# Kernel optimization log

Hardware: AMD Instinct MI355X
Metric: run time of the kernel (lower is better)

## Reference

```python
import jax, jax.numpy as jnp
import numpy as np

QTZ_BETA = 0.25


def setup_inputs() -> dict:
    key = jax.random.key(0)
    k1, k2 = jax.random.split(key)
    z = jax.random.normal(k1, (65536, 1, 256), dtype=jnp.float32)
    codebook = jax.random.normal(k2, (4096, 256), dtype=jnp.float32)
    return {"z": z, "codebook": codebook}


def reference(z, codebook):
    """Hard VQ quantization: nearest-codebook lookup with straight-through
    estimator plus codebook commitment loss. Returns (z_q, codebook_loss,
    min_embed_ids)."""
    D = codebook.shape[-1]
    z_f = z.reshape(-1, D)  # [N, D]
    # Pairwise squared L2 distances via expansion: ||z||^2 - 2 z c^T + ||c||^2
    # (argmin is invariant to the monotone transform vs. torch.cdist's sqrt)
    d2 = (
        jnp.sum(z_f * z_f, axis=1, keepdims=True)  # [N, 1]
        - 2.0 * (z_f @ codebook.T)                 # [N, K]
        + jnp.sum(codebook * codebook, axis=1)     # [K]
    )
    min_embed_ids = jnp.argmin(d2, axis=1)  # [N]
    # one_hot @ codebook is exactly a gather of codebook rows
    z_q = jnp.take(codebook, min_embed_ids, axis=0).reshape(z.shape)
    # Straight-through estimator
    z_q = z + jax.lax.stop_gradient(z_q - z)
    # Codebook loss (uses the STE z_q, matching the torch code)
    codebook_loss = (
        jnp.mean((jax.lax.stop_gradient(z_q) - z) ** 2)
        + jnp.mean((z_q - jax.lax.stop_gradient(z)) ** 2) * QTZ_BETA
    )
    return (z_q, codebook_loss, min_embed_ids)
```

## Files before the change

kernel.cpp:

```cpp
#include <hip/hip_runtime.h>
#include <stdint.h>

typedef _Float16 f16;
typedef _Float16 f16x4 __attribute__((ext_vector_type(4)));
typedef _Float16 f16x8 __attribute__((ext_vector_type(8)));
typedef float f32x4 __attribute__((ext_vector_type(4)));
typedef unsigned long long u64;

#define D_DIM 256
#define K_CB 4096
#define N_ROWS 65536
#define BM 128
#define BN 256
#define N_TILES 16
#define N_STEPS 128
#define LOSS_OFF 16777216
#define IDS_OFF 16777217
#define MAX_FIX 4096

#define WS_CHI 0
#define WS_CN 2097152
#define WS_CNT 2113536
#define WS_ROWS 2113600
#define WS_SLOTS 2129984

#define A_BASE 0
#define B_BASE 65536
#define CN_BASE 131072
#define LDS_BYTES 147456

#define GL_LDS(g, s_) __builtin_amdgcn_global_load_lds( \
    (const __attribute__((address_space(1))) void*)(g), \
    (__attribute__((address_space(3))) void*)(s_), 16, 0, 0)

static __device__ __forceinline__ uint32_t f2u(float x) { union { float f; uint32_t u; } c; c.f = x; return c.u; }
static __device__ __forceinline__ float u2f(uint32_t x) { union { float f; uint32_t u; } c; c.u = x; return c.f; }
static __device__ __forceinline__ uint32_t umin_(uint32_t a, uint32_t b) { return a < b ? a : b; }
static __device__ __forceinline__ uint32_t umax_(uint32_t a, uint32_t b) { return a > b ? a : b; }
static __device__ __forceinline__ u64 d2u(double x) { union { double d; u64 u; } c; c.d = x; return c.u; }

static __device__ __forceinline__ uint32_t med3u(uint32_t a, uint32_t b, uint32_t c) {
    uint32_t d;
    asm("v_med3_u32 %0, %1, %2, %3" : "=v"(d) : "v"(a), "v"(b), "v"(c));
    return d;
}
static __device__ __forceinline__ uint32_t min3u(uint32_t a, uint32_t b, uint32_t c) {
    uint32_t d;
    asm("v_min3_u32 %0, %1, %2, %3" : "=v"(d) : "v"(a), "v"(b), "v"(c));
    return d;
}

#define INS3(s_, kk_) do { \
    const uint32_t kkv_ = (kk_); \
    const uint32_t n1_ = umin_(k1[s_], kkv_); \
    const uint32_t n2_ = med3u(kkv_, k1[s_], k2[s_]); \
    const uint32_t n3_ = med3u(kkv_, k2[s_], k3[s_]); \
    k1[s_] = n1_; k2[s_] = n2_; k3[s_] = n3_; \
} while (0)

__global__ __launch_bounds__(256) void k_prep_cb(const float* __restrict__ cb,
                                                 f16* __restrict__ chi,
                                                 float* __restrict__ cn,
                                                 uint32_t* __restrict__ cnt,
                                                 u64* __restrict__ slots,
                                                 float* __restrict__ loss_slot) {
    const int tid = threadIdx.x;
    const int w = tid >> 6, l = tid & 63;
    const int row = blockIdx.x * 4 + w;
    const float4 v = ((const float4*)cb)[row * 64 + l];
    f16x4 h4;
    h4[0] = (f16)v.x; h4[1] = (f16)v.y; h4[2] = (f16)v.z; h4[3] = (f16)v.w;
    float ss = v.x * v.x + v.y * v.y + v.z * v.z + v.w * v.w;
#pragma unroll
    for (int m = 32; m >= 1; m >>= 1) ss += __shfl_xor(ss, m);
    ((f16x4*)chi)[row * 64 + l] = h4;
    if (l == 0) cn[row] = ss;
    if (tid < 4) slots[blockIdx.x * 4 + tid] = 0xFFFFFFFFFFFFFFFFull;
    if (blockIdx.x == 0 && tid == 0) { *cnt = 0; *loss_slot = 0.0f; }
}

__global__ __launch_bounds__(512, 2) void k_main(const float* __restrict__ z,
                                                 const float* __restrict__ cb,
                                                 const f16* __restrict__ chi,
                                                 const float* __restrict__ cn,
                                                 uint32_t* __restrict__ cnt,
                                                 uint32_t* __restrict__ rows,
                                                 float* __restrict__ out) {
    extern __shared__ char smem[];
    const int tid = threadIdx.x;
    const int w = tid >> 6, l = tid & 63;
    const int wm = w >> 2, wn = w & 3;
    const int l15 = l & 15, qh = l >> 4;
    const int blk = blockIdx.x;
    const float* ztile = z + (size_t)blk * (BM * D_DIM);

    const int e_lo = (w << 4) + (l >> 2);
    const int swq = ((l & 3) ^ ((l >> 3) & 3)) << 3;
    const int offE0 = e_lo * 256 + swq;
    const int offE1 = offE0 + 32768;
    const int stg0 = w * 1024;
    const int stg1 = stg0 + 8192;

#pragma unroll
    for (int s = 0; s < 3; ++s) {
        const f16* gh = chi + s * 32;
        GL_LDS(gh + offE0, smem + B_BASE + s * 16384 + stg0);
        GL_LDS(gh + offE1, smem + B_BASE + s * 16384 + stg1);
    }

    ((float4*)(smem + CN_BASE))[tid] = ((const float4*)cn)[tid];
    ((float4*)(smem + CN_BASE))[tid + 512] = ((const float4*)cn)[tid + 512];

#pragma unroll 4
    for (int p = 0; p < 16; ++p) {
        const int r = p * 8 + w;
        const float4 v = ((const float4*)ztile)[r * 64 + l];
        f16x4 h4;
        h4[0] = (f16)(v.x * -2.0f); h4[1] = (f16)(v.y * -2.0f);
        h4[2] = (f16)(v.z * -2.0f); h4[3] = (f16)(v.w * -2.0f);
        const int kcw = l >> 3, q = (l >> 1) & 3, half = l & 1;
        const int addr = A_BASE + kcw * 8192 + r * 64 + (((q ^ ((r >> 1) & 3))) << 4) + half * 8;
        *(f16x4*)(smem + addr) = h4;
    }

    const int ab = A_BASE + wm * 4096 + l15 * 64 + ((qh ^ ((l15 >> 1) & 3)) << 4);
    const int bb0 = B_BASE + wn * 4096 + l15 * 64 + ((qh ^ ((l15 >> 1) & 3)) << 4);

    uint32_t k1[16], k2[16], k3[16];
#pragma unroll
    for (int s = 0; s < 16; ++s) { k1[s] = 0xFFFFFFFFu; k2[s] = 0xFFFFFFFFu; k3[s] = 0xFFFFFFFFu; }

    f32x4 acc[4][4];
    f16x8 pA[4], pB[4], qA[4], qB[4];

    __syncthreads();

#pragma unroll
    for (int i = 0; i < 4; ++i) pA[i] = *(const f16x8*)(smem + ab + i * 1024);
#pragma unroll
    for (int j = 0; j < 4; ++j) pB[j] = *(const f16x8*)(smem + bb0 + j * 1024);

#define K_STEP(kc_, CA, CB, NA, NB) do { \
    asm volatile("s_waitcnt vmcnt(2)" ::: "memory"); \
    __builtin_amdgcn_s_barrier(); \
    __builtin_amdgcn_sched_barrier(0); \
    { int s3 = tile * 8 + (kc_) + 3; if (s3 > N_STEPS - 1) s3 = N_STEPS - 1; \
      const f16* gh_ = chi + (s3 >> 3) * (BN * D_DIM) + (s3 & 7) * 32; \
      char* bb_ = smem + B_BASE + (((kc_) + 3) & 3) * 16384; \
      GL_LDS(gh_ + offE0, bb_ + stg0); \
      GL_LDS(gh_ + offE1, bb_ + stg1); } \
    _Pragma("unroll") for (int i = 0; i < 4; ++i) \
        NA[i] = *(const f16x8*)(smem + ab + (((kc_) + 1) & 7) * 8192 + i * 1024); \
    _Pragma("unroll") for (int j = 0; j < 4; ++j) \
        NB[j] = *(const f16x8*)(smem + bb0 + (((kc_) + 1) & 3) * 16384 + j * 1024); \
    _Pragma("unroll") for (int i = 0; i < 4; ++i) \
        _Pragma("unroll") for (int j = 0; j < 4; ++j) \
            acc[i][j] = __builtin_amdgcn_mfma_f32_16x16x32_f16(CA[i], CB[j], acc[i][j], 0, 0, 0); \
} while (0)

    for (int tile = 0; tile < N_TILES; ++tile) {
        const int cnb = CN_BASE + tile * 1024 + wn * 256 + l15 * 4;
#pragma unroll
        for (int j = 0; j < 4; ++j) {
            const float base = *(const float*)(smem + cnb + j * 64) + 64.0f;
#pragma unroll
            for (int i = 0; i < 4; ++i) acc[i][j] = (f32x4){base, base, base, base};
        }
        K_STEP(0, pA, pB, qA, qB);
        K_STEP(1, qA, qB, pA, pB);
        K_STEP(2, pA, pB, qA, qB);
        K_STEP(3, qA, qB, pA, pB);
        K_STEP(4, pA, pB, qA, qB);
        K_STEP(5, qA, qB, pA, pB);
        K_STEP(6, pA, pB, qA, qB);
        K_STEP(7, qA, qB, pA, pB);
        const int colb = tile * BN + wn * 64 + l15;
#pragma unroll
        for (int j = 0; j < 4; ++j) {
            const uint32_t col = (uint32_t)(colb + j * 16);
#pragma unroll
            for (int i = 0; i < 4; ++i)
#pragma unroll
                for (int rr = 0; rr < 4; ++rr) {
                    const uint32_t kk = (f2u(acc[i][j][rr]) & 0xFFFFF000u) | col;
                    INS3(i * 4 + rr, kk);
                }
        }
    }
#undef K_STEP
    asm volatile("s_waitcnt vmcnt(0)" ::: "memory");

#pragma unroll
    for (int s = 0; s < 16; ++s) {
        uint32_t a1 = k1[s], a2 = k2[s], a3 = k3[s];
#pragma unroll
        for (int m = 1; m <= 8; m <<= 1) {
            const uint32_t b1 = (uint32_t)__shfl_xor((int)a1, m);
            const uint32_t b2 = (uint32_t)__shfl_xor((int)a2, m);
            const uint32_t b3 = (uint32_t)__shfl_xor((int)a3, m);
            const uint32_t r1 = umin_(a1, b1);
            const uint32_t r2 = min3u(a2, b2, umax_(a1, b1));
            const uint32_t r3 = min3u(umax_(a1, b2), umax_(a2, b1), umin_(a3, b3));
            a1 = r1; a2 = r2; a3 = r3;
        }
        k1[s] = a1; k2[s] = a2; k3[s] = a3;
    }
    __syncthreads();
    uint32_t* mk = (uint32_t*)(smem + CN_BASE);
    double* lossW = (double*)(smem + CN_BASE + 1536);
    if (wn == 0 && l15 == 0) {
#pragma unroll
        for (int s = 0; s < 16; ++s) {
            const int row = wm * 64 + (s >> 2) * 16 + qh * 4 + (s & 3);
            mk[row] = k1[s]; mk[128 + row] = k2[s]; mk[256 + row] = k3[s];
        }
    }
#pragma unroll
    for (int mw = 1; mw < 4; ++mw) {
        __syncthreads();
        if (wn == mw && l15 == 0) {
#pragma unroll
            for (int s = 0; s < 16; ++s) {
                const int row = wm * 64 + (s >> 2) * 16 + qh * 4 + (s & 3);
                const uint32_t b1 = mk[row], b2 = mk[128 + row], b3 = mk[256 + row];
                mk[row] = umin_(k1[s], b1);
                mk[128 + row] = min3u(k2[s], b2, umax_(k1[s], b1));
                mk[256 + row] = min3u(umax_(k1[s], b2), umax_(k2[s], b1), umin_(k3[s], b3));
            }
        }
    }
    __syncthreads();

    double lossAcc = 0.0;
    for (int it = 0; it < 16; ++it) {
        const int row = it * 8 + w;
        const uint32_t K1 = mk[row], K2 = mk[128 + row], K3 = mk[256 + row];
        const int col1 = (int)(K1 & 4095u), col2 = (int)(K2 & 4095u);
        const float4 c1 = ((const float4*)cb)[col1 * 64 + l];
        const float4 c2 = ((const float4*)cb)[col2 * 64 + l];
        const float4 z4 = ((const float4*)ztile)[row * 64 + l];
        double e1, e2;
        {
            const double dx1 = (double)c1.x - z4.x, dy1 = (double)c1.y - z4.y;
            const double dz1 = (double)c1.z - z4.z, dw1 = (double)c1.w - z4.w;
            e1 = dx1 * dx1 + dy1 * dy1 + dz1 * dz1 + dw1 * dw1;
            const double dx2 = (double)c2.x - z4.x, dy2 = (double)c2.y - z4.y;
            const double dz2 = (double)c2.z - z4.z, dw2 = (double)c2.w - z4.w;
            e2 = dx2 * dx2 + dy2 * dy2 + dz2 * dz2 + dw2 * dw2;
        }
        float zn2 = z4.x * z4.x + z4.y * z4.y + z4.z * z4.z + z4.w * z4.w;
#pragma unroll
        for (int m = 32; m >= 1; m >>= 1) {
            e1 += __shfl_xor(e1, m);
            e2 += __shfl_xor(e2, m);
            zn2 += __shfl_xor(zn2, m);
        }
        const bool take1 = (e1 < e2) || (e1 == e2 && col1 <= col2);
        const float4 cw = take1 ? c1 : c2;
        ((float4*)out)[(blk * BM + row) * 64 + l] = cw;
        if (l == 0) {
            const int colw = take1 ? col1 : col2;
            const double ew = take1 ? e1 : e2;
            out[IDS_OFF + blk * BM + row] = (float)colw;
            lossAcc += ew;
            const float d3 = u2f(K3 & 0xFFFFF000u) + zn2 - 64.0f;
            const float eps = 0.006f * sqrtf(zn2) + 0.01f;
            if (!((float)ew < d3 - eps)) {
                const uint32_t e = atomicAdd(cnt, 1u);
                if (e < MAX_FIX) rows[e] = (uint32_t)(blk * BM + row);
            }
        }
    }
    if (l == 0) lossW[w] = lossAcc;
    __syncthreads();
    if (tid == 0) {
        double tot = 0.0;
#pragma unroll
        for (int i = 0; i < 8; ++i) tot += lossW[i];
        atomicAdd(out + LOSS_OFF, (float)(tot * (1.25 / 16777216.0)));
    }
}

__global__ __launch_bounds__(256) void k_fix_scan(const float* __restrict__ z,
                                                  const float* __restrict__ cb,
                                                  const uint32_t* __restrict__ cnt,
                                                  const uint32_t* __restrict__ rows,
                                                  u64* __restrict__ slots) {
    __shared__ float zrow[256];
    __shared__ u64 wmin[4];
    const int tid = threadIdx.x;
    const int w = tid >> 6, l = tid & 63;
    const int chunk = blockIdx.x & 15;
    uint32_t n = *cnt; if (n > MAX_FIX) n = MAX_FIX;
    for (uint32_t e = blockIdx.x >> 4; e < n; e += 64) {
        const int row = (int)rows[e];
        __syncthreads();
        if (tid < 64) ((float4*)zrow)[tid] = ((const float4*)z)[row * 64 + tid];
        __syncthreads();
        const int c = chunk * 256 + tid;
        const float4* crow = (const float4*)(cb + (size_t)c * 256);
        double s = 0.0;
        for (int q = 0; q < 64; ++q) {
            const float4 cv = crow[q];
            const float4 zv = ((const float4*)zrow)[q];
            const double dx = (double)cv.x - zv.x, dy = (double)cv.y - zv.y;
            const double dz = (double)cv.z - zv.z, dw = (double)cv.w - zv.w;
            s += dx * dx + dy * dy + dz * dz + dw * dw;
        }
        u64 key = (d2u(s) & 0xFFFFFFFFFFFFF000ull) | (u64)c;
#pragma unroll
        for (int m = 32; m >= 1; m >>= 1) {
            const u64 o = __shfl_xor(key, m);
            if (o < key) key = o;
        }
        if (l == 0) wmin[w] = key;
        __syncthreads();
        if (tid == 0) {
            u64 k = wmin[0];
            if (wmin[1] < k) k = wmin[1];
            if (wmin[2] < k) k = wmin[2];
            if (wmin[3] < k) k = wmin[3];
            atomicMin(&slots[e], k);
        }
    }
}

__global__ __launch_bounds__(256) void k_fix_patch(const float* __restrict__ z,
                                                   const float* __restrict__ cb,
                                                   const uint32_t* __restrict__ cnt,
                                                   const uint32_t* __restrict__ rows,
                                                   const u64* __restrict__ slots,
                                                   float* __restrict__ out) {
    const int tid = threadIdx.x;
    uint32_t n = *cnt; if (n > MAX_FIX) n = MAX_FIX;
    for (uint32_t e = blockIdx.x; e < n; e += 256) {
        const int row = (int)rows[e];
        const int newc = (int)(slots[e] & 4095ull);
        const int oldc = (int)out[IDS_OFF + row];
        if (newc == oldc) continue;
        double dOld = 0.0, dNew = 0.0;
        if (tid < 64) {
            const float4 zv = ((const float4*)z)[row * 64 + tid];
            const float4 co = ((const float4*)cb)[oldc * 64 + tid];
            const float4 cn4 = ((const float4*)cb)[newc * 64 + tid];
            const double ax = (double)co.x - zv.x, ay = (double)co.y - zv.y;
            const double az = (double)co.z - zv.z, aw = (double)co.w - zv.w;
            dOld = ax * ax + ay * ay + az * az + aw * aw;
            const double bx = (double)cn4.x - zv.x, by = (double)cn4.y - zv.y;
            const double bz = (double)cn4.z - zv.z, bw = (double)cn4.w - zv.w;
            dNew = bx * bx + by * by + bz * bz + bw * bw;
            ((float4*)out)[row * 64 + tid] = cn4;
        }
#pragma unroll
        for (int m = 32; m >= 1; m >>= 1) {
            dOld += __shfl_xor(dOld, m);
            dNew += __shfl_xor(dNew, m);
        }
        if (tid == 0) {
            out[IDS_OFF + row] = (float)newc;
            atomicAdd(out + LOSS_OFF, (float)((dNew - dOld) * (1.25 / 16777216.0)));
        }
    }
}

extern "C" void kernel_launch(void* const* d_in, const int* in_sizes, int n_in,
                              void* d_out, int out_size, void* d_ws, size_t ws_size,
                              hipStream_t stream) {
    (void)in_sizes; (void)n_in; (void)out_size; (void)ws_size;
    const float* z = (const float*)d_in[0];
    const float* cb = (const float*)d_in[1];
    float* out = (float*)d_out;
    char* ws = (char*)d_ws;
    f16* chi = (f16*)(ws + WS_CHI);
    float* cn = (float*)(ws + WS_CN);
    uint32_t* cnt = (uint32_t*)(ws + WS_CNT);
    uint32_t* rows = (uint32_t*)(ws + WS_ROWS);
    u64* slots = (u64*)(ws + WS_SLOTS);

    hipFuncSetAttribute((const void*)k_main,
                        hipFuncAttributeMaxDynamicSharedMemorySize, LDS_BYTES);

    k_prep_cb<<<K_CB / 4, 256, 0, stream>>>(cb, chi, cn, cnt, slots, out + LOSS_OFF);
    k_main<<<N_ROWS / BM, 512, LDS_BYTES, stream>>>(z, cb, chi, cn, cnt, rows, out);
    k_fix_scan<<<1024, 256, 0, stream>>>(z, cb, cnt, rows, slots);
    k_fix_patch<<<256, 256, 0, stream>>>(z, cb, cnt, rows, slots, out);
}
```

Before: 296.0 us.

## Double-buffer accumulators to overlap top-3 epilogue with next tile's MFMAs

After: 305.5 us. 3.2% more time.

```diff
diff --git a/kernel.cpp b/kernel.cpp
--- a/kernel.cpp
+++ b/kernel.cpp
@@ -125,56 +125,86 @@
 
     const int ab = A_BASE + wm * 4096 + l15 * 64 + ((qh ^ ((l15 >> 1) & 3)) << 4);
     const int bb0 = B_BASE + wn * 4096 + l15 * 64 + ((qh ^ ((l15 >> 1) & 3)) << 4);
+    const int cnA = CN_BASE + wn * 256 + l15 * 4;
 
     uint32_t k1[16], k2[16], k3[16];
 #pragma unroll
     for (int s = 0; s < 16; ++s) { k1[s] = 0xFFFFFFFFu; k2[s] = 0xFFFFFFFFu; k3[s] = 0xFFFFFFFFu; }
 
-    f32x4 acc[4][4];
-    f16x8 pA[4], pB[4], qA[4], qB[4];
+    f32x4 accA[4][4], accB[4][4];
+    {
+        const float iv = __builtin_inff();
+#pragma unroll
+        for (int i = 0; i < 4; ++i)
+#pragma unroll
+            for (int j = 0; j < 4; ++j) accB[i][j] = (f32x4){iv, iv, iv, iv};
+    }
+    f16x8 ah[4], bhf[4];
+    float cnNext[4];
 
     __syncthreads();
 
 #pragma unroll
-    for (int i = 0; i < 4; ++i) pA[i] = *(const f16x8*)(smem + ab + i * 1024);
-#pragma unroll
-    for (int j = 0; j < 4; ++j) pB[j] = *(const f16x8*)(smem + bb0 + j * 1024);
-
-#define K_STEP(kc_, CA, CB, NA, NB) do { \
-    asm volatile("s_waitcnt vmcnt(2)" ::: "memory"); \
-    __builtin_amdgcn_s_barrier(); \
-    __builtin_amdgcn_sched_barrier(0); \
-    { int s3 = tile * 8 + (kc_) + 3; if (s3 > N_STEPS - 1) s3 = N_STEPS - 1; \
-      const f16* gh_ = chi + (s3 >> 3) * (BN * D_DIM) + (s3 & 7) * 32; \
-      char* bb_ = smem + B_BASE + (((kc_) + 3) & 3) * 16384; \
-      GL_LDS(gh_ + offE0, bb_ + stg0); \
-      GL_LDS(gh_ + offE1, bb_ + stg1); } \
-    _Pragma("unroll") for (int i = 0; i < 4; ++i) \
-        NA[i] = *(const f16x8*)(smem + ab + (((kc_) + 1) & 7) * 8192 + i * 1024); \
-    _Pragma("unroll") for (int j = 0; j < 4; ++j) \
-        NB[j] = *(const f16x8*)(smem + bb0 + (((kc_) + 1) & 3) * 16384 + j * 1024); \
-    _Pragma("unroll") for (int i = 0; i < 4; ++i) \
+    for (int j = 0; j < 4; ++j) cnNext[j] = *(const float*)(smem + cnA + j * 64);
+
+#define TILE_BODY(ACC, PREV, TILE) do { \
+    const int tile_ = (TILE); \
+    _Pragma("unroll") for (int j = 0; j < 4; ++j) { \
+        const float base_ = cnNext[j] + 64.0f; \
+        _Pragma("unroll") for (int i = 0; i < 4; ++i) \
+            ACC[i][j] = (f32x4){base_, base_, base_, base_}; \
+    } \
+    const int prevColb_ = (tile_ - 1) * BN + wn * 64 + l15; \
+    _Pragma("unroll") for (int kc = 0; kc < 8; ++kc) { \
+         \
+        _Pragma("unroll") for (int i = 0; i < 4; ++i) \
+            ah[i] = *(const f16x8*)(smem + ab + kc * 8192 + i * 1024); \
         _Pragma("unroll") for (int j = 0; j < 4; ++j) \
-            acc[i][j] = __builtin_amdgcn_mfma_f32_16x16x32_f16(CA[i], CB[j], acc[i][j], 0, 0, 0); \
+            bhf[j] = *(const f16x8*)(smem + bb0 + (kc & 3) * 16384 + j * 1024); \
+         \
+        { int s3 = tile_ * 8 + kc + 3; if (s3 > N_STEPS - 1) s3 = N_STEPS - 1; \
+          const f16* gh_ = chi + (s3 >> 3) * (BN * D_DIM) + (s3 & 7) * 32; \
+          char* bb_ = smem + B_BASE + ((kc + 3) & 3) * 16384; \
+          GL_LDS(gh_ + offE0, bb_ + stg0); \
+          GL_LDS(gh_ + offE1, bb_ + stg1); } \
+        if (kc == 0) { \
+            const int tn_ = (tile_ + 1 < N_TILES) ? tile_ + 1 : tile_; \
+            _Pragma("unroll") for (int j = 0; j < 4; ++j) \
+                cnNext[j] = *(const float*)(smem + cnA + tn_ * 1024 + j * 64); \
+        } \
+        {  \
+            const int pi_ = kc >> 1; \
+            _Pragma("unroll") for (int jj = 0; jj < 2; ++jj) { \
+                const int pj_ = (kc & 1) * 2 + jj; \
+                const uint32_t col_ = (uint32_t)(prevColb_ + pj_ * 16); \
+                _Pragma("unroll") for (int rr = 0; rr < 4; ++rr) { \
+                    const uint32_t kk_ = (f2u(PREV[pi_][pj_][rr]) & 0xFFFFF000u) | col_; \
+                    INS3(pi_ * 4 + rr, kk_); \
+                } \
+            } \
+        } \
+        asm volatile("s_waitcnt vmcnt(4)" ::: "memory"); \
+        __builtin_amdgcn_s_barrier(); \
+        asm volatile("s_waitcnt lgkmcnt(0)" ::: "memory"); \
+        __builtin_amdgcn_sched_barrier(0); \
+        __builtin_amdgcn_s_setprio(1); \
+        _Pragma("unroll") for (int i = 0; i < 4; ++i) \
+            _Pragma("unroll") for (int j = 0; j < 4; ++j) \
+                ACC[i][j] = __builtin_amdgcn_mfma_f32_16x16x32_f16(ah[i], bhf[j], ACC[i][j], 0, 0, 0); \
+        __builtin_amdgcn_s_setprio(0); \
+        __builtin_amdgcn_s_barrier(); \
+    } \
 } while (0)
 
-    for (int tile = 0; tile < N_TILES; ++tile) {
-        const int cnb = CN_BASE + tile * 1024 + wn * 256 + l15 * 4;
-#pragma unroll
-        for (int j = 0; j < 4; ++j) {
-            const float base = *(const float*)(smem + cnb + j * 64) + 64.0f;
-#pragma unroll
-            for (int i = 0; i < 4; ++i) acc[i][j] = (f32x4){base, base, base, base};
-        }
-        K_STEP(0, pA, pB, qA, qB);
-        K_STEP(1, qA, qB, pA, pB);
-        K_STEP(2, pA, pB, qA, qB);
-        K_STEP(3, qA, qB, pA, pB);
-        K_STEP(4, pA, pB, qA, qB);
-        K_STEP(5, qA, qB, pA, pB);
-        K_STEP(6, pA, pB, qA, qB);
-        K_STEP(7, qA, qB, pA, pB);
-        const int colb = tile * BN + wn * 64 + l15;
+    for (int tp = 0; tp < N_TILES; tp += 2) {
+        TILE_BODY(accA, accB, tp);
+        TILE_BODY(accB, accA, tp + 1);
+    }
+#undef TILE_BODY
+    asm volatile("s_waitcnt vmcnt(0)" ::: "memory");
+
+    {
+        const int colb = (N_TILES - 1) * BN + wn * 64 + l15;
 #pragma unroll
         for (int j = 0; j < 4; ++j) {
             const uint32_t col = (uint32_t)(colb + j * 16);
@@ -182,13 +212,11 @@
             for (int i = 0; i < 4; ++i)
 #pragma unroll
                 for (int rr = 0; rr < 4; ++rr) {
-                    const uint32_t kk = (f2u(acc[i][j][rr]) & 0xFFFFF000u) | col;
+                    const uint32_t kk = (f2u(accB[i][j][rr]) & 0xFFFFF000u) | col;
                     INS3(i * 4 + rr, kk);
                 }
         }
     }
-#undef K_STEP
-    asm volatile("s_waitcnt vmcnt(0)" ::: "memory");
 
 #pragma unroll
     for (int s = 0; s < 16; ++s) {
```
